# Performance work log

Hardware: AMD Instinct MI355X
Metric: run time of the kernel (lower is better)

The kernel has to match this reference:

```python
import jax, jax.numpy as jnp
import numpy as np

N = 100000
E = 1600000
F_IN = 256
H1, C1 = 8, 8          # conv1: 8 heads x 8 channels -> 64
H2, C2 = 1, 32         # conv2: 1 head x num_classes
SLOPE = 0.2


def gat_conv(x, src, dst, n, W, a_src, a_dst, b, heads, out):
    # x: [n, f_in]; W: [f_in, heads*out]; a_src/a_dst: [heads, out]; b: [heads*out]
    h = (x @ W).reshape(n, heads, out)                       # [n, H, C]
    s = jnp.sum(h * a_src, axis=-1)                          # [n, H]
    d = jnp.sum(h * a_dst, axis=-1)                          # [n, H]
    e = jax.nn.leaky_relu(s[src] + d[dst], SLOPE)            # [e, H]
    m = jax.ops.segment_max(e, dst, num_segments=n)          # stable segment softmax
    ex = jnp.exp(e - m[dst])
    z = jax.ops.segment_sum(ex, dst, num_segments=n)
    alpha = ex / (z[dst] + 1e-16)                            # [e, H]
    msg = alpha[:, :, None] * h[src]                         # [e, H, C]
    agg = jax.ops.segment_sum(msg, dst, num_segments=n)      # [n, H, C]
    return agg.reshape(n, heads * out) + b


def setup_inputs() -> dict:
    key = jax.random.key(0)
    ks = jax.random.split(key, 10)
    x = jax.random.normal(ks[0], (N, F_IN), dtype=jnp.float32)
    edge_index = jax.random.randint(ks[1], (2, E), 0, N, dtype=jnp.int32)
    sc = 0.05
    W1 = jax.random.normal(ks[2], (F_IN, H1 * C1), dtype=jnp.float32) * sc
    att_src1 = jax.random.normal(ks[3], (H1, C1), dtype=jnp.float32) * sc
    att_dst1 = jax.random.normal(ks[4], (H1, C1), dtype=jnp.float32) * sc
    b1 = jnp.zeros((H1 * C1,), dtype=jnp.float32)
    W2 = jax.random.normal(ks[5], (H1 * C1, H2 * C2), dtype=jnp.float32) * sc
    att_src2 = jax.random.normal(ks[6], (H2, C2), dtype=jnp.float32) * sc
    att_dst2 = jax.random.normal(ks[7], (H2, C2), dtype=jnp.float32) * sc
    b2 = jnp.zeros((H2 * C2,), dtype=jnp.float32)
    return {"x": x, "edge_index": edge_index, "W1": W1, "att_src1": att_src1,
            "att_dst1": att_dst1, "b1": b1, "W2": W2, "att_src2": att_src2,
            "att_dst2": att_dst2, "b2": b2}


def reference(x, edge_index, W1, att_src1, att_dst1, b1, W2, att_src2, att_dst2, b2):
    # add self loops (PyG GATConv default)
    loops = jnp.arange(N, dtype=edge_index.dtype)
    src = jnp.concatenate([edge_index[0], loops])
    dst = jnp.concatenate([edge_index[1], loops])
    # dropout layers are identity in eval mode
    h = gat_conv(x, src, dst, N, W1, att_src1, att_dst1, b1, H1, C1)
    h = jax.nn.elu(h)
    h = gat_conv(h, src, dst, N, W2, att_src2, att_dst2, b2, H2, C2)
    return jax.nn.log_softmax(h, axis=1)
```

## Files before the change

kernel.cpp:

```cpp
#include <hip/hip_runtime.h>
#include <hip/hip_bf16.h>

#define N_NODES 100000
#define N_EDGES 1600000
#define N_TOT   (N_EDGES + N_NODES)
#define F_IN    256
#define F1      64
#define H1      8
#define C1      8
#define F2      32
#define SLOPE   0.2f

#define NB_G    ((N_NODES + 255) / 256)
#define NB_X    3125

#define EB      4096
#define NB1     ((N_EDGES + EB - 1) / EB)
#define BW      256
#define NBKT    ((N_NODES + BW - 1) / BW)

typedef unsigned int  uint;
typedef unsigned short ushort;
typedef __attribute__((ext_vector_type(8))) short bf16x8;
typedef __attribute__((ext_vector_type(4))) float f32x4;
typedef __attribute__((ext_vector_type(2))) float f32x2;

__device__ inline ushort f2bf(float f) {
    uint u = __float_as_uint(f);
    uint r = u + 0x7fffu + ((u >> 16) & 1u);
    return (ushort)(r >> 16);
}
__device__ inline float bflo(uint u) { return __uint_as_float(u << 16); }
__device__ inline float bfhi(uint u) { return __uint_as_float(u & 0xffff0000u); }
__device__ inline uint pk2bf(float a, float b) {
    __hip_bfloat162 h = __float22bfloat162_rn(make_float2(a, b));
    union { __hip_bfloat162 h; uint u; } cv; cv.h = h;
    return cv.u;
}

__device__ inline void bucket_bases(const int* __restrict__ colsum,
                                    int* sc, int* sb, int tid) {
    const int i0 = 2 * tid, i1 = 2 * tid + 1;
    const int a0 = (i0 < NBKT) ? colsum[i0] : 0;
    const int a1 = (i1 < NBKT) ? colsum[i1] : 0;
    sc[tid] = a0 + a1;
    __syncthreads();
    for (int off = 1; off < 256; off <<= 1) {
        int t = (tid >= off) ? sc[tid - off] : 0;
        __syncthreads();
        sc[tid] += t;
        __syncthreads();
    }
    const int excl = sc[tid] - (a0 + a1);
    if (i0 < NBKT)  sb[i0] = excl;
    if (i1 <= NBKT) sb[i1] = excl + a0;
    __syncthreads();
}

__global__ __launch_bounds__(256) void k_p1w(
        const int* __restrict__ ei, const float* __restrict__ W1,
        const float* __restrict__ x,
        int* __restrict__ bcnt, ushort* __restrict__ w1b,
        ushort* __restrict__ xb) {
    __shared__ int H[NBKT];
    const int tid = threadIdx.x;
    if (blockIdx.x < NB_X) {
        const size_t base = (size_t)blockIdx.x * 8192;
#pragma unroll
        for (int r = 0; r < 8; ++r) {
            const size_t idx = base + (size_t)r * 1024 + tid * 4;
            const float4 v = *(const float4*)(x + idx);
            *(uint2*)(xb + idx) = make_uint2(pk2bf(v.x, v.y), pk2bf(v.z, v.w));
        }
        return;
    }
    if (blockIdx.x == NB_X) {
        for (int i = 0; i < 64; ++i) {
            const int e = i * 256 + tid;
            const int k = e >> 6, n = e & 63;
            w1b[((k >> 3) * 64 + n) * 8 + (k & 7)] = f2bf(W1[e]);
        }
        return;
    }
    const int blk = blockIdx.x - NB_X - 1;
    for (int j = tid; j < NBKT; j += 256) H[j] = 0;
    __syncthreads();
    const int e0 = blk * EB;
    const int lim = (e0 + EB < N_EDGES) ? e0 + EB : N_EDGES;
    for (int i = e0 + tid * 2; i < lim; i += 512) {
        const int2 dd = *(const int2*)&ei[N_EDGES + i];
        atomicAdd(&H[dd.x >> 8], 1);
        atomicAdd(&H[dd.y >> 8], 1);
    }
    __syncthreads();
    for (int j = tid; j < NBKT; j += 256)
        bcnt[j * NB1 + blk] = H[j];
}

__global__ __launch_bounds__(64) void k_p2(
        int* __restrict__ bcnt, int* __restrict__ colsum) {
    const int col = blockIdx.x, lane = threadIdx.x;
    int carry = 0;
    for (int c0 = 0; c0 < NB1; c0 += 64) {
        const int idx = c0 + lane;
        const int v = (idx < NB1) ? bcnt[col * NB1 + idx] : 0;
        int s = v;
#pragma unroll
        for (int off = 1; off < 64; off <<= 1) {
            int u = __shfl_up(s, off);
            if (lane >= off) s += u;
        }
        if (idx < NB1) bcnt[col * NB1 + idx] = carry + s - v;
        carry += __shfl(s, 63);
    }
    if (lane == 0) colsum[col] = carry;
}

__global__ __launch_bounds__(256) void k_p3(
        const int* __restrict__ ei, const int* __restrict__ bcnt,
        const int* __restrict__ colsum, uint* __restrict__ tmp) {
    __shared__ int sc[256];
    __shared__ int cur[NBKT + 1];
    const int tid = threadIdx.x, blk = blockIdx.x;
    bucket_bases(colsum, sc, cur, tid);
    for (int b = tid; b < NBKT; b += 256) cur[b] += bcnt[b * NB1 + blk];
    __syncthreads();
    const int e0 = blk * EB;
    const int lim = (e0 + EB < N_EDGES) ? e0 + EB : N_EDGES;
    for (int i = e0 + tid * 2; i < lim; i += 512) {
        const int2 ss = *(const int2*)&ei[i];
        const int2 dd = *(const int2*)&ei[N_EDGES + i];
        const int p0 = atomicAdd(&cur[dd.x >> 8], 1);
        tmp[p0] = ((uint)(dd.x & 255) << 24) | (uint)ss.x;
        const int p1 = atomicAdd(&cur[dd.y >> 8], 1);
        tmp[p1] = ((uint)(dd.y & 255) << 24) | (uint)ss.y;
    }
}

__global__ __launch_bounds__(256) void k_final_gemm(
        const uint* __restrict__ tmp, const int* __restrict__ colsum,
        int* __restrict__ row_ptr, int* __restrict__ srcs,
        const ushort* __restrict__ xb, const ushort* __restrict__ w1b,
        const float* __restrict__ as1, const float* __restrict__ ad1,
        ushort* __restrict__ h1b, float* __restrict__ s1,
        float* __restrict__ d1) {
    __shared__ union {
        struct { int sc[256]; int sb[NBKT + 1]; int cur[BW]; } f;
        ushort B[F_IN * F1];
        ushort S[4][64][66];
    } sm;
    const int tid = threadIdx.x;

    if (blockIdx.x < NBKT) {
        const int b = blockIdx.x;
        bucket_bases(colsum, sm.f.sc, sm.f.sb, tid);
        sm.f.cur[tid] = 0;
        __syncthreads();
        const int lo = sm.f.sb[b], hi = sm.f.sb[b + 1];
        for (int i = lo + tid; i < hi; i += 256)
            atomicAdd(&sm.f.cur[tmp[i] >> 24], 1);
        __syncthreads();
        const int n = b * BW + tid;
        const int myc = sm.f.cur[tid];
        const int v = (n < N_NODES) ? myc + 1 : 0;
        __syncthreads();
        sm.f.sc[tid] = v;
        __syncthreads();
        for (int off = 1; off < 256; off <<= 1) {
            int t = (tid >= off) ? sm.f.sc[tid - off] : 0;
            __syncthreads();
            sm.f.sc[tid] += t;
            __syncthreads();
        }
        const int rp = lo + b * BW + (sm.f.sc[tid] - v);
        if (n < N_NODES) {
            row_ptr[n] = rp;
            srcs[rp] = n;
        }
        if (b == NBKT - 1 && tid == 255) row_ptr[N_NODES] = N_TOT;
        sm.f.cur[tid] = rp + 1;
        __syncthreads();
        for (int i = lo + tid; i < hi; i += 256) {
            const uint u = tmp[i];
            const int pos = atomicAdd(&sm.f.cur[u >> 24], 1);
            srcs[pos] = (int)(u & 0xFFFFFFu);
        }
        return;
    }

    {
        const uint4* s4 = (const uint4*)w1b;
        uint4* d4 = (uint4*)sm.B;
#pragma unroll
        for (int i = 0; i < 8; ++i)
            d4[i * 256 + tid] = s4[i * 256 + tid];
    }
    __syncthreads();

    const int wave = tid >> 6, lane = tid & 63;
    const int q = lane >> 4, ln = lane & 15;
    const int rowbase = (blockIdx.x - NBKT) * 256 + wave * 64;

    f32x4 acc[4][4];
#pragma unroll
    for (int mt = 0; mt < 4; ++mt)
#pragma unroll
        for (int nt = 0; nt < 4; ++nt) acc[mt][nt] = (f32x4){0.f, 0.f, 0.f, 0.f};

    const ushort* xrow[4];
#pragma unroll
    for (int mt = 0; mt < 4; ++mt) {
        const int r = rowbase + mt * 16 + ln;
        const int rc = r < N_NODES ? r : N_NODES - 1;
        xrow[mt] = xb + (size_t)rc * F_IN + q * 8;
    }

#pragma unroll 4
    for (int t = 0; t < 8; ++t) {
        bf16x8 bfr[4];
#pragma unroll
        for (int nt = 0; nt < 4; ++nt)
            bfr[nt] = *(const bf16x8*)&sm.B[((t * 4 + q) * 64 + nt * 16 + ln) * 8];
        bf16x8 af[4];
#pragma unroll
        for (int mt = 0; mt < 4; ++mt)
            af[mt] = *(const bf16x8*)(xrow[mt] + t * 32);
#pragma unroll
        for (int mt = 0; mt < 4; ++mt)
#pragma unroll
            for (int nt = 0; nt < 4; ++nt)
                acc[mt][nt] = __builtin_amdgcn_mfma_f32_16x16x32_bf16(
                                  af[mt], bfr[nt], acc[mt][nt], 0, 0, 0);
    }
    __syncthreads();

#pragma unroll
    for (int mt = 0; mt < 4; ++mt)
#pragma unroll
        for (int nt = 0; nt < 4; ++nt)
#pragma unroll
            for (int r = 0; r < 4; ++r)
                sm.S[wave][mt * 16 + q * 4 + r][nt * 16 + ln] = f2bf(acc[mt][nt][r]);
    __syncthreads();

    const int node = rowbase + lane;
    if (node >= N_NODES) return;
    const uint* srow = (const uint*)&sm.S[wave][lane][0];
    float sacc[H1], dacc[H1];
#pragma unroll
    for (int h = 0; h < H1; ++h) { sacc[h] = 0.f; dacc[h] = 0.f; }
    uint4* hout = (uint4*)(h1b + (size_t)node * F1);
#pragma unroll
    for (int p4 = 0; p4 < 8; ++p4) {
        const uint u0 = srow[p4 * 4 + 0], u1 = srow[p4 * 4 + 1];
        const uint u2 = srow[p4 * 4 + 2], u3 = srow[p4 * 4 + 3];
        hout[p4] = make_uint4(u0, u1, u2, u3);
        const float c[8] = {bflo(u0), bfhi(u0), bflo(u1), bfhi(u1),
                            bflo(u2), bfhi(u2), bflo(u3), bfhi(u3)};
#pragma unroll
        for (int j = 0; j < 8; ++j) {
            sacc[p4] += c[j] * as1[p4 * 8 + j];
            dacc[p4] += c[j] * ad1[p4 * 8 + j];
        }
    }
    float4* s4 = (float4*)(s1 + (size_t)node * H1);
    float4* d4 = (float4*)(d1 + (size_t)node * H1);
    s4[0] = make_float4(sacc[0], sacc[1], sacc[2], sacc[3]);
    s4[1] = make_float4(sacc[4], sacc[5], sacc[6], sacc[7]);
    d4[0] = make_float4(dacc[0], dacc[1], dacc[2], dacc[3]);
    d4[1] = make_float4(dacc[4], dacc[5], dacc[6], dacc[7]);
}

__global__ __launch_bounds__(256) void k_agg1(
        const int* __restrict__ row_ptr, const int* __restrict__ srcs,
        const ushort* __restrict__ h1b, const float* __restrict__ s1,
        const float* __restrict__ d1, const float* __restrict__ b1,
        const float* __restrict__ W2, const float* __restrict__ as2,
        const float* __restrict__ ad2,
        ushort* __restrict__ h2b, float* __restrict__ s2,
        float* __restrict__ d2) {
    __shared__ float sx[4][64];
    const int wid = (blockIdx.x * 256 + threadIdx.x) >> 6;
    if (wid >= N_NODES) return;
    const int w = threadIdx.x >> 6;
    const int lane = threadIdx.x & 63;
    const int q = lane >> 2;
    const int cp = lane & 3;
    const float2 dh2 = *(const float2*)((const char*)d1 + (size_t)wid * 32 + 8 * cp);
    const int beg = row_ptr[wid], end = row_ptr[wid + 1];
    const char* hP = (const char*)h1b;
    const char* sP = (const char*)s1;
    const uint hOff = 32u * (uint)cp;
    const uint sOff = 8u * (uint)cp;
    f32x2 A0 = {0.f, 0.f}, A1 = {0.f, 0.f}, A2 = {0.f, 0.f}, A3 = {0.f, 0.f};
    f32x2 A4 = {0.f, 0.f}, A5 = {0.f, 0.f}, A6 = {0.f, 0.f}, A7 = {0.f, 0.f};
    f32x2 z2 = {0.f, 0.f};
    for (int i = beg + q; i < end; i += 16) {
        const int nA = srcs[i];
        const float2 sv2 = *(const float2*)(sP + ((uint)nA * 32u + sOff));
        float e0 = sv2.x + dh2.x, e1 = sv2.y + dh2.y;
        e0 = fmaxf(e0, SLOPE * e0);
        e1 = fmaxf(e1, SLOPE * e1);
        const float x0 = __expf(e0), x1 = __expf(e1);
        const uint base = (uint)nA * 128u + hOff;
        const uint4 U0 = *(const uint4*)(hP + base);
        const uint4 U1 = *(const uint4*)(hP + base + 16);
        z2 += (f32x2){x0, x1};
        const f32x2 xa0 = {x0, x0}, xa1 = {x1, x1};
        A0 += xa0 * (f32x2){bflo(U0.x), bfhi(U0.x)};
        A1 += xa0 * (f32x2){bflo(U0.y), bfhi(U0.y)};
        A2 += xa0 * (f32x2){bflo(U0.z), bfhi(U0.z)};
        A3 += xa0 * (f32x2){bflo(U0.w), bfhi(U0.w)};
        A4 += xa1 * (f32x2){bflo(U1.x), bfhi(U1.x)};
        A5 += xa1 * (f32x2){bflo(U1.y), bfhi(U1.y)};
        A6 += xa1 * (f32x2){bflo(U1.z), bfhi(U1.z)};
        A7 += xa1 * (f32x2){bflo(U1.w), bfhi(U1.w)};
    }
    f32x2 r0, r1, r2, r3;
    float zf;
    {
        const bool hi = lane & 4;
        f32x2 s0 = hi ? A0 : A4, s1v = hi ? A1 : A5;
        f32x2 s2v = hi ? A2 : A6, s3v = hi ? A3 : A7;
        const f32x2 k0 = hi ? A4 : A0, k1 = hi ? A5 : A1;
        const f32x2 k2 = hi ? A6 : A2, k3 = hi ? A7 : A3;
        s0.x = __shfl_xor(s0.x, 4); s0.y = __shfl_xor(s0.y, 4);
        s1v.x = __shfl_xor(s1v.x, 4); s1v.y = __shfl_xor(s1v.y, 4);
        s2v.x = __shfl_xor(s2v.x, 4); s2v.y = __shfl_xor(s2v.y, 4);
        s3v.x = __shfl_xor(s3v.x, 4); s3v.y = __shfl_xor(s3v.y, 4);
        r0 = k0 + s0; r1 = k1 + s1v; r2 = k2 + s2v; r3 = k3 + s3v;
        float zs = hi ? z2.x : z2.y;
        const float zk = hi ? z2.y : z2.x;
        zs = __shfl_xor(zs, 4);
        zf = zk + zs;
    }
    {
        const bool hi = lane & 8;
        f32x2 s0 = hi ? r0 : r2, s1v = hi ? r1 : r3;
        const f32x2 k0 = hi ? r2 : r0, k1 = hi ? r3 : r1;
        s0.x = __shfl_xor(s0.x, 8); s0.y = __shfl_xor(s0.y, 8);
        s1v.x = __shfl_xor(s1v.x, 8); s1v.y = __shfl_xor(s1v.y, 8);
        r0 = k0 + s0; r1 = k1 + s1v;
    }
    {
        const bool hi = lane & 16;
        f32x2 s0 = hi ? r0 : r1;
        const f32x2 k0 = hi ? r1 : r0;
        s0.x = __shfl_xor(s0.x, 16); s0.y = __shfl_xor(s0.y, 16);
        r0 = k0 + s0;
    }
    float sv;
    {
        const bool hi = lane & 32;
        float s0 = hi ? r0.x : r0.y;
        const float k0 = hi ? r0.y : r0.x;
        s0 = __shfl_xor(s0, 32);
        sv = k0 + s0;
    }
    zf += __shfl_xor(zf, 8); zf += __shfl_xor(zf, 16); zf += __shfl_xor(zf, 32);

    const int xi = cp * 16 + ((lane >> 2) & 1) * 8 + ((lane >> 3) & 1) * 4
                 + ((lane >> 4) & 1) * 2 + ((lane >> 5) & 1);
    const float zi = 1.f / (zf + 1e-16f);
    float xv = sv * zi + b1[xi];
    xv = xv > 0.f ? xv : __expf(xv) - 1.f;
    sx[w][xi] = xv;
    __builtin_amdgcn_wave_barrier();

    const int kh = lane >> 5;
    const int oc = lane & 31;
    const float4* sxv = (const float4*)&sx[w][kh * 32];
    const float* wp0 = W2 + (size_t)(kh * 32) * F2 + oc;
    float acc = 0.f;
#pragma unroll
    for (int k4 = 0; k4 < 8; ++k4) {
        const float4 xv4 = sxv[k4];
        const float* wp = wp0 + (size_t)k4 * 4 * F2;
        acc += xv4.x * wp[0]      + xv4.y * wp[F2]
             + xv4.z * wp[2 * F2] + xv4.w * wp[3 * F2];
    }
    acc += __shfl_xor(acc, 32);

    float sA2 = acc * as2[oc], dA2 = acc * ad2[oc];
#pragma unroll
    for (int off = 1; off <= 16; off <<= 1) {
        sA2 += __shfl_xor(sA2, off);
        dA2 += __shfl_xor(dA2, off);
    }
    const float accp = __shfl_xor(acc, 1);
    if (lane < 32 && !(lane & 1))
        *(uint*)&h2b[(size_t)wid * F2 + oc] = pk2bf(acc, accp);
    if (lane == 0) { s2[wid] = sA2; d2[wid] = dA2; }
}

__global__ __launch_bounds__(256) void k_agg2(
        const int* __restrict__ row_ptr, const int* __restrict__ srcs,
        const ushort* __restrict__ h2b, const float* __restrict__ s2,
        const float* __restrict__ d2, const float* __restrict__ b2,
        float* __restrict__ out) {
    const int wid = (blockIdx.x * 256 + threadIdx.x) >> 6;
    if (wid >= N_NODES) return;
    const int lane = threadIdx.x & 63;
    const int q = lane >> 1;
    const int ch = lane & 1;
    const float dn = d2[wid];
    const int beg = row_ptr[wid], end = row_ptr[wid + 1];
    const char* hP = (const char*)h2b;
    const char* sP = (const char*)s2;
    const uint ch32 = 32u * (uint)ch;
    f32x2 A0 = {0.f, 0.f}, A1 = {0.f, 0.f}, A2 = {0.f, 0.f}, A3 = {0.f, 0.f};
    f32x2 A4 = {0.f, 0.f}, A5 = {0.f, 0.f}, A6 = {0.f, 0.f}, A7 = {0.f, 0.f};
    float z = 0.f;
    for (int i = beg + q; i < end; i += 32) {
        const int nA = srcs[i];
        float eA = *(const float*)(sP + (uint)nA * 4u) + dn;
        eA = fmaxf(eA, SLOPE * eA);
        const float xA = __expf(eA);
        const uint off = (uint)nA * 64u + ch32;
        const uint4 U0 = *(const uint4*)(hP + off);
        const uint4 U1 = *(const uint4*)(hP + off + 16);
        z += xA;
        const f32x2 xa = {xA, xA};
        A0 += xa * (f32x2){bflo(U0.x), bfhi(U0.x)};
        A1 += xa * (f32x2){bflo(U0.y), bfhi(U0.y)};
        A2 += xa * (f32x2){bflo(U0.z), bfhi(U0.z)};
        A3 += xa * (f32x2){bflo(U0.w), bfhi(U0.w)};
        A4 += xa * (f32x2){bflo(U1.x), bfhi(U1.x)};
        A5 += xa * (f32x2){bflo(U1.y), bfhi(U1.y)};
        A6 += xa * (f32x2){bflo(U1.z), bfhi(U1.z)};
        A7 += xa * (f32x2){bflo(U1.w), bfhi(U1.w)};
    }
    f32x2 r0, r1, r2, r3;
    {
        const bool hi = lane & 2;
        f32x2 s0 = hi ? A0 : A4, s1v = hi ? A1 : A5;
        f32x2 s2v = hi ? A2 : A6, s3v = hi ? A3 : A7;
        const f32x2 k0 = hi ? A4 : A0, k1 = hi ? A5 : A1;
        const f32x2 k2 = hi ? A6 : A2, k3 = hi ? A7 : A3;
        s0.x = __shfl_xor(s0.x, 2); s0.y = __shfl_xor(s0.y, 2);
        s1v.x = __shfl_xor(s1v.x, 2); s1v.y = __shfl_xor(s1v.y, 2);
        s2v.x = __shfl_xor(s2v.x, 2); s2v.y = __shfl_xor(s2v.y, 2);
        s3v.x = __shfl_xor(s3v.x, 2); s3v.y = __shfl_xor(s3v.y, 2);
        r0 = k0 + s0; r1 = k1 + s1v; r2 = k2 + s2v; r3 = k3 + s3v;
    }
    {
        const bool hi = lane & 4;
        f32x2 s0 = hi ? r0 : r2, s1v = hi ? r1 : r3;
        const f32x2 k0 = hi ? r2 : r0, k1 = hi ? r3 : r1;
        s0.x = __shfl_xor(s0.x, 4); s0.y = __shfl_xor(s0.y, 4);
        s1v.x = __shfl_xor(s1v.x, 4); s1v.y = __shfl_xor(s1v.y, 4);
        r0 = k0 + s0; r1 = k1 + s1v;
    }
    {
        const bool hi = lane & 8;
        f32x2 s0 = hi ? r0 : r1;
        const f32x2 k0 = hi ? r1 : r0;
        s0.x = __shfl_xor(s0.x, 8); s0.y = __shfl_xor(s0.y, 8);
        r0 = k0 + s0;
    }
    float sv;
    {
        const bool hi = lane & 16;
        float s0 = hi ? r0.x : r0.y;
        const float k0 = hi ? r0.y : r0.x;
        s0 = __shfl_xor(s0, 16);
        sv = k0 + s0;
    }
    sv += __shfl_xor(sv, 32);
    z += __shfl_xor(z, 2); z += __shfl_xor(z, 4); z += __shfl_xor(z, 8);
    z += __shfl_xor(z, 16); z += __shfl_xor(z, 32);

    const int elem = ch * 16 + ((lane >> 1) & 1) * 8 + ((lane >> 2) & 1) * 4
                   + ((lane >> 3) & 1) * 2 + ((lane >> 4) & 1);
    const float zi = 1.f / (z + 1e-16f);
    const float v = sv * zi + b2[elem];
    float m = v;
#pragma unroll
    for (int off = 1; off <= 16; off <<= 1) m = fmaxf(m, __shfl_xor(m, off));
    float ssum = __expf(v - m);
#pragma unroll
    for (int off = 1; off <= 16; off <<= 1) ssum += __shfl_xor(ssum, off);
    const float lse = m + __logf(ssum);
    if (lane < 32) out[(size_t)wid * F2 + elem] = v - lse;
}

extern "C" void kernel_launch(void* const* d_in, const int* in_sizes, int n_in,
                              void* d_out, int out_size, void* d_ws, size_t ws_size,
                              hipStream_t stream) {
    const float* x   = (const float*)d_in[0];
    const int*   ei  = (const int*)d_in[1];
    const float* W1  = (const float*)d_in[2];
    const float* as1 = (const float*)d_in[3];
    const float* ad1 = (const float*)d_in[4];
    const float* b1  = (const float*)d_in[5];
    const float* W2  = (const float*)d_in[6];
    const float* as2 = (const float*)d_in[7];
    const float* ad2 = (const float*)d_in[8];
    const float* b2  = (const float*)d_in[9];
    float* out = (float*)d_out;

    ushort* xb  = (ushort*)d_ws;
    ushort* h1b = xb + (size_t)N_NODES * F_IN;
    ushort* h2b = h1b + (size_t)N_NODES * F1;
    ushort* w1b = h2b + (size_t)N_NODES * F2;
    float*  s1  = (float*)(w1b + F_IN * F1);
    float*  d1  = s1 + (size_t)N_NODES * H1;
    float*  s2  = d1 + (size_t)N_NODES * H1;
    float*  d2  = s2 + N_NODES;
    uint*   tmp = (uint*)(d2 + N_NODES);
    int* row_ptr = (int*)(tmp + N_EDGES);
    int* colsum  = row_ptr + N_NODES + 1;
    int* bcnt    = colsum + NBKT;
    int* srcs    = bcnt + (size_t)NBKT * NB1;

    const int nb_w = (N_NODES * 64 + 255) / 256;

    k_p1w<<<NB_X + 1 + NB1, 256, 0, stream>>>(ei, W1, x, bcnt, w1b, xb);
    k_p2<<<NBKT, 64, 0, stream>>>(bcnt, colsum);
    k_p3<<<NB1, 256, 0, stream>>>(ei, bcnt, colsum, tmp);
    k_final_gemm<<<NBKT + NB_G, 256, 0, stream>>>(tmp, colsum, row_ptr, srcs,
                                                  xb, w1b, as1, ad1,
                                                  h1b, s1, d1);
    k_agg1<<<nb_w, 256, 0, stream>>>(row_ptr, srcs, h1b, s1, d1, b1,
                                     W2, as2, ad2, h2b, s2, d2);
    k_agg2<<<nb_w, 256, 0, stream>>>(row_ptr, srcs, h2b, s2, d2, b2, out);
}
```

Baseline: 344.1 us.

## Fuse x-to-bf16 conversion into layer-1 GEMM and shrink GEMM tile per wave

Drops the separate pass that converts x (100k×256 fp32) into a bf16 workspace copy. The GEMM now reads fp32 x directly and packs it to bf16 in registers, which removes one full write and re-read of the converted matrix. The GEMM tile is reduced to 16 rows per wave, 64 rows per block, and W1 fragments are read straight from global/L2 instead of being staged in LDS. The cost is more blocks, less reuse of W1 per wave, and only 16 of 64 lanes doing the per-node epilogue.

```diff
diff --git a/kernel.cpp b/kernel.cpp
--- a/kernel.cpp
+++ b/kernel.cpp
@@ -11,8 +11,7 @@
 #define F2      32
 #define SLOPE   0.2f
 
-#define NB_G    ((N_NODES + 255) / 256)
-#define NB_X    3125
+#define NB_G2   ((N_NODES + 63) / 64)
 
 #define EB      4096
 #define NB1     ((N_EDGES + EB - 1) / EB)
@@ -59,22 +58,10 @@
 
 __global__ __launch_bounds__(256) void k_p1w(
         const int* __restrict__ ei, const float* __restrict__ W1,
-        const float* __restrict__ x,
-        int* __restrict__ bcnt, ushort* __restrict__ w1b,
-        ushort* __restrict__ xb) {
+        int* __restrict__ bcnt, ushort* __restrict__ w1b) {
     __shared__ int H[NBKT];
     const int tid = threadIdx.x;
-    if (blockIdx.x < NB_X) {
-        const size_t base = (size_t)blockIdx.x * 8192;
-#pragma unroll
-        for (int r = 0; r < 8; ++r) {
-            const size_t idx = base + (size_t)r * 1024 + tid * 4;
-            const float4 v = *(const float4*)(x + idx);
-            *(uint2*)(xb + idx) = make_uint2(pk2bf(v.x, v.y), pk2bf(v.z, v.w));
-        }
-        return;
-    }
-    if (blockIdx.x == NB_X) {
+    if (blockIdx.x == NB1) {
         for (int i = 0; i < 64; ++i) {
             const int e = i * 256 + tid;
             const int k = e >> 6, n = e & 63;
@@ -82,7 +69,7 @@
         }
         return;
     }
-    const int blk = blockIdx.x - NB_X - 1;
+    const int blk = blockIdx.x;
     for (int j = tid; j < NBKT; j += 256) H[j] = 0;
     __syncthreads();
     const int e0 = blk * EB;
@@ -140,14 +127,13 @@
 __global__ __launch_bounds__(256) void k_final_gemm(
         const uint* __restrict__ tmp, const int* __restrict__ colsum,
         int* __restrict__ row_ptr, int* __restrict__ srcs,
-        const ushort* __restrict__ xb, const ushort* __restrict__ w1b,
+        const float* __restrict__ x, const ushort* __restrict__ w1b,
         const float* __restrict__ as1, const float* __restrict__ ad1,
         ushort* __restrict__ h1b, float* __restrict__ s1,
         float* __restrict__ d1) {
     __shared__ union {
         struct { int sc[256]; int sb[NBKT + 1]; int cur[BW]; } f;
-        ushort B[F_IN * F1];
-        ushort S[4][64][66];
+        ushort S[4][16][66];
     } sm;
     const int tid = threadIdx.x;
 
@@ -188,61 +174,42 @@
         return;
     }
 
-    {
-        const uint4* s4 = (const uint4*)w1b;
-        uint4* d4 = (uint4*)sm.B;
-#pragma unroll
-        for (int i = 0; i < 8; ++i)
-            d4[i * 256 + tid] = s4[i * 256 + tid];
-    }
-    __syncthreads();
-
     const int wave = tid >> 6, lane = tid & 63;
     const int q = lane >> 4, ln = lane & 15;
-    const int rowbase = (blockIdx.x - NBKT) * 256 + wave * 64;
-
-    f32x4 acc[4][4];
-#pragma unroll
-    for (int mt = 0; mt < 4; ++mt)
-#pragma unroll
-        for (int nt = 0; nt < 4; ++nt) acc[mt][nt] = (f32x4){0.f, 0.f, 0.f, 0.f};
-
-    const ushort* xrow[4];
-#pragma unroll
-    for (int mt = 0; mt < 4; ++mt) {
-        const int r = rowbase + mt * 16 + ln;
-        const int rc = r < N_NODES ? r : N_NODES - 1;
-        xrow[mt] = xb + (size_t)rc * F_IN + q * 8;
-    }
+    const int rowbase = (blockIdx.x - NBKT) * 64 + wave * 16;
+    const int row = rowbase + ln;
+    const int rowc = row < N_NODES ? row : N_NODES - 1;
+    const float* xr = x + (size_t)rowc * F_IN + q * 8;
+
+    f32x4 acc[4];
+#pragma unroll
+    for (int nt = 0; nt < 4; ++nt) acc[nt] = (f32x4){0.f, 0.f, 0.f, 0.f};
 
 #pragma unroll 4
     for (int t = 0; t < 8; ++t) {
+        const float4 a0 = *(const float4*)(xr + t * 32);
+        const float4 a1 = *(const float4*)(xr + t * 32 + 4);
+        uint4 au = make_uint4(pk2bf(a0.x, a0.y), pk2bf(a0.z, a0.w),
+                              pk2bf(a1.x, a1.y), pk2bf(a1.z, a1.w));
+        bf16x8 af = *(bf16x8*)&au;
         bf16x8 bfr[4];
 #pragma unroll
         for (int nt = 0; nt < 4; ++nt)
-            bfr[nt] = *(const bf16x8*)&sm.B[((t * 4 + q) * 64 + nt * 16 + ln) * 8];
-        bf16x8 af[4];
-#pragma unroll
-        for (int mt = 0; mt < 4; ++mt)
-            af[mt] = *(const bf16x8*)(xrow[mt] + t * 32);
-#pragma unroll
-        for (int mt = 0; mt < 4; ++mt)
-#pragma unroll
-            for (int nt = 0; nt < 4; ++nt)
-                acc[mt][nt] = __builtin_amdgcn_mfma_f32_16x16x32_bf16(
-                                  af[mt], bfr[nt], acc[mt][nt], 0, 0, 0);
-    }
-    __syncthreads();
-
-#pragma unroll
-    for (int mt = 0; mt < 4; ++mt)
+            bfr[nt] = *(const bf16x8*)&w1b[((t * 4 + q) * 64 + nt * 16 + ln) * 8];
 #pragma unroll
         for (int nt = 0; nt < 4; ++nt)
-#pragma unroll
-            for (int r = 0; r < 4; ++r)
-                sm.S[wave][mt * 16 + q * 4 + r][nt * 16 + ln] = f2bf(acc[mt][nt][r]);
-    __syncthreads();
-
+            acc[nt] = __builtin_amdgcn_mfma_f32_16x16x32_bf16(
+                          af, bfr[nt], acc[nt], 0, 0, 0);
+    }
+
+#pragma unroll
+    for (int nt = 0; nt < 4; ++nt)
+#pragma unroll
+        for (int r = 0; r < 4; ++r)
+            sm.S[wave][q * 4 + r][nt * 16 + ln] = f2bf(acc[nt][r]);
+    __builtin_amdgcn_wave_barrier();
+
+    if (lane >= 16) return;
     const int node = rowbase + lane;
     if (node >= N_NODES) return;
     const uint* srow = (const uint*)&sm.S[wave][lane][0];
@@ -499,8 +466,7 @@
     const float* b2  = (const float*)d_in[9];
     float* out = (float*)d_out;
 
-    ushort* xb  = (ushort*)d_ws;
-    ushort* h1b = xb + (size_t)N_NODES * F_IN;
+    ushort* h1b = (ushort*)d_ws;
     ushort* h2b = h1b + (size_t)N_NODES * F1;
     ushort* w1b = h2b + (size_t)N_NODES * F2;
     float*  s1  = (float*)(w1b + F_IN * F1);
@@ -515,12 +481,12 @@
 
     const int nb_w = (N_NODES * 64 + 255) / 256;
 
-    k_p1w<<<NB_X + 1 + NB1, 256, 0, stream>>>(ei, W1, x, bcnt, w1b, xb);
+    k_p1w<<<NB1 + 1, 256, 0, stream>>>(ei, W1, bcnt, w1b);
     k_p2<<<NBKT, 64, 0, stream>>>(bcnt, colsum);
     k_p3<<<NB1, 256, 0, stream>>>(ei, bcnt, colsum, tmp);
-    k_final_gemm<<<NBKT + NB_G, 256, 0, stream>>>(tmp, colsum, row_ptr, srcs,
-                                                  xb, w1b, as1, ad1,
-                                                  h1b, s1, d1);
+    k_final_gemm<<<NBKT + NB_G2, 256, 0, stream>>>(tmp, colsum, row_ptr, srcs,
+                                                   x, w1b, as1, ad1,
+                                                   h1b, s1, d1);
     k_agg1<<<nb_w, 256, 0, stream>>>(row_ptr, srcs, h1b, s1, d1, b1,
                                      W2, as2, ad2, h2b, s2, d2);
     k_agg2<<<nb_w, 256, 0, stream>>>(row_ptr, srcs, h2b, s2, d2, b2, out);
```

Result: faster. 333.8 us (-3.0%).
